# Optimization experiments

Measured on AMD Instinct MI355X. Metric: run time of the kernel, lower is better.

Reference implementation:

```python
import jax, jax.numpy as jnp
import numpy as np

D_IN = 1024
D_OUT = 1024
N_HEADS = 16
D_HEAD = D_OUT // N_HEADS


def setup_inputs() -> dict:
    key = jax.random.key(0)
    ks = jax.random.split(key, 6)
    s = 0.02
    return {
        "x": jax.random.normal(ks[0], (4, 2048, D_IN), dtype=jnp.float32),
        "wq": jax.random.normal(ks[1], (D_IN, D_OUT), dtype=jnp.float32) * s,
        "wk": jax.random.normal(ks[2], (D_IN, D_OUT), dtype=jnp.float32) * s,
        "wv": jax.random.normal(ks[3], (D_IN, D_OUT), dtype=jnp.float32) * s,
        "wo": jax.random.normal(ks[4], (D_OUT, D_OUT), dtype=jnp.float32) * s,
        "bo": jax.random.normal(ks[5], (D_OUT,), dtype=jnp.float32) * s,
    }


def reference(x, wq, wk, wv, wo, bo):
    B, T, _ = x.shape
    # QKV projections (no bias), split into heads: (B, H, T, Dh)
    def split_heads(t):
        return t.reshape(B, T, N_HEADS, D_HEAD).transpose(0, 2, 1, 3)
    q = split_heads(x @ wq)
    k = split_heads(x @ wk)
    v = split_heads(x @ wv)
    # attention scores (B, H, T, T), causal mask, scale by sqrt(d_head)
    scores = jnp.einsum("bhqd,bhkd->bhqk", q, k)
    causal = jnp.tril(jnp.ones((T, T), dtype=bool))
    scores = jnp.where(causal, scores, -jnp.inf)
    attn = jax.nn.softmax(scores / jnp.sqrt(jnp.float32(D_HEAD)), axis=-1)
    # dropout = 0.0 (eval) -> identity
    ctx = jnp.einsum("bhqk,bhkd->bhqd", attn, v)
    ctx = ctx.transpose(0, 2, 1, 3).reshape(B, T, D_OUT)
    return ctx @ wo + bo
```

## Files before the change

### kernel.cpp

```cpp
#include <hip/hip_runtime.h>
#include <stdint.h>


typedef unsigned short u16;
typedef __bf16 bf16x8 __attribute__((ext_vector_type(8)));
typedef float f32x4 __attribute__((ext_vector_type(4)));

__device__ __forceinline__ u16 f2bf(float f) {
  union { float f; unsigned u; } v; v.f = f;
  return (u16)((v.u + 0x7fffu + ((v.u >> 16) & 1u)) >> 16);
}

__device__ __forceinline__ void gl_lds16(const void* g, void* l) {
  __builtin_amdgcn_global_load_lds((__attribute__((address_space(1))) void*)g,
                                   (__attribute__((address_space(3))) void*)l,
                                   16, 0, 0);
}

__global__ __launch_bounds__(256) void conv_x_k(const float* __restrict__ x,
                                                u16* __restrict__ xb) {
  int i = (blockIdx.x * 256 + threadIdx.x) * 4;
  float4 v = *reinterpret_cast<const float4*>(x + i);
  ushort4 o;
  o.x = f2bf(v.x); o.y = f2bf(v.y); o.z = f2bf(v.z); o.w = f2bf(v.w);
  *reinterpret_cast<ushort4*>(xb + i) = o;
}

__global__ __launch_bounds__(256) void conv_w_k(const float* __restrict__ w0,
                                                const float* __restrict__ w1,
                                                const float* __restrict__ w2,
                                                const float* __restrict__ w3,
                                                u16* __restrict__ dst) {
  const float* src = blockIdx.z == 0 ? w0 : blockIdx.z == 1 ? w1
                   : blockIdx.z == 2 ? w2 : w3;
  u16* d = dst + (size_t)blockIdx.z * 1024 * 1024;
  __shared__ float tile[32][33];
  int n0 = blockIdx.x * 32, k0 = blockIdx.y * 32;
  int tx = threadIdx.x & 31, ty = threadIdx.x >> 5;
  #pragma unroll
  for (int r = 0; r < 32; r += 8)
    tile[ty + r][tx] = src[(k0 + ty + r) * 1024 + n0 + tx];
  __syncthreads();
  #pragma unroll
  for (int r = 0; r < 32; r += 8)
    d[(n0 + ty + r) * 1024 + k0 + tx] = f2bf(tile[tx][ty + r]);
}

#define GSW(base, row, chunk) \
  ((char*)(base) + (row) * 64 + ((((chunk) ^ (((row) >> 1) & 3))) << 4))

__global__ __launch_bounds__(256) void gemm_qkv_k(const u16* __restrict__ A,
                                                  const u16* __restrict__ Wt,
                                                  u16* __restrict__ qw,
                                                  u16* __restrict__ kw,
                                                  u16* __restrict__ vtw) {
  __shared__ u16 SM[16384];
  const int tid = threadIdx.x;
  const int wave = tid >> 6, lane = tid & 63;
  const int quad = lane >> 4, l15 = lane & 15;
  const int m0 = blockIdx.x * 128;
  const int which = blockIdx.y >> 3;
  const int n0 = (blockIdx.y & 7) * 128;
  const u16* Bt = Wt + which * (1024 * 1024);
  const int waveM = (wave >> 1) * 64, waveN = (wave & 1) * 64;

  const f32x4 fz = {0.f, 0.f, 0.f, 0.f};
  f32x4 acc[4][4];
  #pragma unroll
  for (int i = 0; i < 4; i++)
    #pragma unroll
    for (int j = 0; j < 4; j++) acc[i][j] = fz;

  const int grow = tid >> 2;
  const int gsw8 = (((tid & 3) ^ ((grow >> 1) & 3)) * 8);
  const u16* Ag = A + (m0 + grow) * 1024 + gsw8;
  const u16* Bg = Bt + (n0 + grow) * 1024 + gsw8;

  {
    char* AsB = (char*)&SM[0] + wave * 1024;
    char* BsB = (char*)&SM[8192] + wave * 1024;
    gl_lds16(Ag, AsB);       gl_lds16(Ag + 65536, AsB + 4096);
    gl_lds16(Bg, BsB);       gl_lds16(Bg + 65536, BsB + 4096);
  }

  for (int s = 0; s < 32; s++) {
    const int cur = (s & 1) * 4096;
    __syncthreads();
    if (s < 31) {
      const int k0 = (s + 1) * 32;
      const int nxt = 4096 - cur;
      char* AsB = (char*)&SM[nxt] + wave * 1024;
      char* BsB = (char*)&SM[8192 + nxt] + wave * 1024;
      gl_lds16(Ag + k0, AsB);      gl_lds16(Ag + 65536 + k0, AsB + 4096);
      gl_lds16(Bg + k0, BsB);      gl_lds16(Bg + 65536 + k0, BsB + 4096);
    }
    bf16x8 af[4], bf[4];
    #pragma unroll
    for (int mi = 0; mi < 4; mi++)
      af[mi] = *reinterpret_cast<const bf16x8*>(GSW(&SM[cur], waveM + mi * 16 + l15, quad));
    #pragma unroll
    for (int ni = 0; ni < 4; ni++)
      bf[ni] = *reinterpret_cast<const bf16x8*>(GSW(&SM[8192 + cur], waveN + ni * 16 + l15, quad));
    #pragma unroll
    for (int mi = 0; mi < 4; mi++)
      #pragma unroll
      for (int ni = 0; ni < 4; ni++)
        acc[mi][ni] = __builtin_amdgcn_mfma_f32_16x16x32_bf16(af[mi], bf[ni], acc[mi][ni], 0, 0, 0);
  }

  if (which != 2) {
    #pragma unroll
    for (int mi = 0; mi < 4; mi++) {
      #pragma unroll
      for (int r = 0; r < 4; r++) {
        int m = m0 + waveM + mi * 16 + quad * 4 + r;
        int b = m >> 11, t = m & 2047;
        #pragma unroll
        for (int ni = 0; ni < 4; ni++) {
          int n = n0 + waveN + ni * 16 + l15;
          int h = n >> 6, d = n & 63;
          float v = acc[mi][ni][r];
          if (which == 0) qw[((b * 16 + h) * 2048 + t) * 64 + d] = f2bf(v * 0.125f);
          else            kw[((b * 16 + h) * 2048 + t) * 64 + d] = f2bf(v);
        }
      }
    }
  } else {
    __syncthreads();
    #pragma unroll
    for (int mi = 0; mi < 4; mi++)
      #pragma unroll
      for (int r = 0; r < 4; r++) {
        int ml = waveM + mi * 16 + quad * 4 + r;
        #pragma unroll
        for (int ni = 0; ni < 4; ni++) {
          int nl = waveN + ni * 16 + l15;
          int byte = nl * 256 + (((ml >> 3) ^ (nl & 7)) << 4) + (ml & 7) * 2;
          *(u16*)((char*)SM + byte) = f2bf(acc[mi][ni][r]);
        }
      }
    __syncthreads();
    const int b = m0 >> 11, t0 = m0 & 2047;
    #pragma unroll
    for (int i = 0; i < 8; i++) {
      int cid = tid + 256 * i;
      int nl = cid >> 4, tc = cid & 15;
      bf16x8 vv = *reinterpret_cast<const bf16x8*>(
          (char*)SM + nl * 256 + ((tc ^ (nl & 7)) << 4));
      int n = n0 + nl;
      int h = n >> 6, d = n & 63;
      *reinterpret_cast<bf16x8*>(vtw + (((b * 16 + h) * 64 + d) * 2048 + t0 + tc * 8)) = vv;
    }
  }
}

__global__ __launch_bounds__(256) void attn_k(const u16* __restrict__ Q,
                                              const u16* __restrict__ K,
                                              const u16* __restrict__ Vt,
                                              u16* __restrict__ ctx) {
  __shared__ u16 QPs[64 * 64];
  __shared__ u16 Ks[2][64 * 64];
  __shared__ u16 Vs[2][64 * 64];
  const int tid = threadIdx.x;
  const int wave = tid >> 6, lane = tid & 63;
  const int quad = lane >> 4, l15 = lane & 15;
  const int bh = blockIdx.x;
  const int qt = 31 - (int)blockIdx.y;
  const int b = bh >> 4, h = bh & 15;

  const u16* Qg = Q + (bh * 2048 + qt * 64) * 64;
  const u16* Kg = K + bh * (2048 * 64);
  const u16* Vg = Vt + bh * (64 * 2048);

  const int lrow = tid >> 3;
  const int lsw = ((tid & 7) ^ (lrow & 7)) * 8;

  gl_lds16(Qg + lrow * 64 + lsw, (char*)QPs + wave * 1024);
  gl_lds16(Qg + (32 + lrow) * 64 + lsw, (char*)QPs + wave * 1024 + 4096);
  {
    char* KsB = (char*)Ks[0] + wave * 1024;
    char* VsB = (char*)Vs[0] + wave * 1024;
    gl_lds16(Kg + lrow * 64 + lsw, KsB);
    gl_lds16(Kg + (32 + lrow) * 64 + lsw, KsB + 4096);
    gl_lds16(Vg + lrow * 2048 + lsw, VsB);
    gl_lds16(Vg + (32 + lrow) * 2048 + lsw, VsB + 4096);
  }

  bf16x8 onesb;
  #pragma unroll
  for (int i = 0; i < 8; i++) onesb[i] = (__bf16)1.0f;

  const f32x4 fz = {0.f, 0.f, 0.f, 0.f};
  f32x4 accO[4];
  f32x4 accL = fz;
  #pragma unroll
  for (int dt = 0; dt < 4; dt++) accO[dt] = fz;
  bf16x8 qf[2];

  #define SWZB(row, chunk) ((row) * 128 + (((chunk) ^ ((row) & 7)) << 4))

  for (int j = 0; j <= qt; j++) {
    const int cur = j & 1;
    __syncthreads();
    if (j < qt) {
      char* KsB = (char*)Ks[cur ^ 1] + wave * 1024;
      char* VsB = (char*)Vs[cur ^ 1] + wave * 1024;
      const int jr = (j + 1) * 64;
      gl_lds16(Kg + (jr + lrow) * 64 + lsw, KsB);
      gl_lds16(Kg + (jr + 32 + lrow) * 64 + lsw, KsB + 4096);
      gl_lds16(Vg + lrow * 2048 + jr + lsw, VsB);
      gl_lds16(Vg + (32 + lrow) * 2048 + jr + lsw, VsB + 4096);
    }
    if (j == 0) {
      #pragma unroll
      for (int kk = 0; kk < 2; kk++)
        qf[kk] = *reinterpret_cast<const bf16x8*>(
            (char*)QPs + SWZB(wave * 16 + l15, kk * 4 + quad));
    }

    f32x4 s[4];
    #pragma unroll
    for (int nt = 0; nt < 4; nt++) s[nt] = fz;
    #pragma unroll
    for (int kk = 0; kk < 2; kk++)
      #pragma unroll
      for (int nt = 0; nt < 4; nt++) {
        bf16x8 kf = *reinterpret_cast<const bf16x8*>(
            (char*)Ks[cur] + SWZB(nt * 16 + l15, kk * 4 + quad));
        s[nt] = __builtin_amdgcn_mfma_f32_16x16x32_bf16(qf[kk], kf, s[nt], 0, 0, 0);
      }

    if (j == qt) {
      #pragma unroll
      for (int nt = 0; nt < 4; nt++) {
        int col = nt * 16 + l15;
        int row0 = wave * 16 + quad * 4;
        #pragma unroll
        for (int r = 0; r < 4; r++)
          if (col > row0 + r) s[nt][r] = -1e30f;
      }
    }

    #pragma unroll
    for (int nt = 0; nt < 4; nt++)
      #pragma unroll
      for (int r = 0; r < 4; r++) {
        int prow = wave * 16 + quad * 4 + r;
        int pcol = nt * 16 + l15;
        int byte = prow * 128 + ((((pcol >> 3) ^ (prow & 7))) << 4) + (pcol & 7) * 2;
        *(u16*)((char*)QPs + byte) = f2bf(__expf(s[nt][r]));
      }
    __asm__ volatile("s_waitcnt lgkmcnt(0)" ::: "memory");

    #pragma unroll
    for (int kk = 0; kk < 2; kk++) {
      bf16x8 pf = *reinterpret_cast<const bf16x8*>(
          (char*)QPs + SWZB(wave * 16 + l15, kk * 4 + quad));
      accL = __builtin_amdgcn_mfma_f32_16x16x32_bf16(pf, onesb, accL, 0, 0, 0);
      #pragma unroll
      for (int dt = 0; dt < 4; dt++) {
        bf16x8 vf = *reinterpret_cast<const bf16x8*>(
            (char*)Vs[cur] + SWZB(dt * 16 + l15, kk * 4 + quad));
        accO[dt] = __builtin_amdgcn_mfma_f32_16x16x32_bf16(pf, vf, accO[dt], 0, 0, 0);
      }
    }
  }
  #undef SWZB

  float inv[4];
  #pragma unroll
  for (int r = 0; r < 4; r++) inv[r] = 1.0f / accL[r];
  const int trow = qt * 64 + wave * 16 + quad * 4;
  #pragma unroll
  for (int dt = 0; dt < 4; dt++)
    #pragma unroll
    for (int r = 0; r < 4; r++)
      ctx[(b * 2048 + trow + r) * 1024 + h * 64 + dt * 16 + l15] =
          f2bf(accO[dt][r] * inv[r]);
}

__global__ __launch_bounds__(256) void gemm_out_k(const u16* __restrict__ A,
                                                  const u16* __restrict__ Wt,
                                                  const float* __restrict__ bo,
                                                  float* __restrict__ out) {
  __shared__ u16 SM[16384];
  const int tid = threadIdx.x;
  const int wave = tid >> 6, lane = tid & 63;
  const int quad = lane >> 4, l15 = lane & 15;
  const int m0 = blockIdx.x * 128;
  const int n0 = blockIdx.y * 128;
  const int waveM = (wave >> 1) * 64, waveN = (wave & 1) * 64;

  const f32x4 fz = {0.f, 0.f, 0.f, 0.f};
  f32x4 acc[4][4];
  #pragma unroll
  for (int i = 0; i < 4; i++)
    #pragma unroll
    for (int j = 0; j < 4; j++) acc[i][j] = fz;

  const int grow = tid >> 2;
  const int gsw8 = (((tid & 3) ^ ((grow >> 1) & 3)) * 8);
  const u16* Ag = A + (m0 + grow) * 1024 + gsw8;
  const u16* Bg = Wt + (n0 + grow) * 1024 + gsw8;

  {
    char* AsB = (char*)&SM[0] + wave * 1024;
    char* BsB = (char*)&SM[8192] + wave * 1024;
    gl_lds16(Ag, AsB);       gl_lds16(Ag + 65536, AsB + 4096);
    gl_lds16(Bg, BsB);       gl_lds16(Bg + 65536, BsB + 4096);
  }

  for (int s = 0; s < 32; s++) {
    const int cur = (s & 1) * 4096;
    __syncthreads();
    if (s < 31) {
      const int k0 = (s + 1) * 32;
      const int nxt = 4096 - cur;
      char* AsB = (char*)&SM[nxt] + wave * 1024;
      char* BsB = (char*)&SM[8192 + nxt] + wave * 1024;
      gl_lds16(Ag + k0, AsB);      gl_lds16(Ag + 65536 + k0, AsB + 4096);
      gl_lds16(Bg + k0, BsB);      gl_lds16(Bg + 65536 + k0, BsB + 4096);
    }
    bf16x8 af[4], bf[4];
    #pragma unroll
    for (int mi = 0; mi < 4; mi++)
      af[mi] = *reinterpret_cast<const bf16x8*>(GSW(&SM[cur], waveM + mi * 16 + l15, quad));
    #pragma unroll
    for (int ni = 0; ni < 4; ni++)
      bf[ni] = *reinterpret_cast<const bf16x8*>(GSW(&SM[8192 + cur], waveN + ni * 16 + l15, quad));
    #pragma unroll
    for (int mi = 0; mi < 4; mi++)
      #pragma unroll
      for (int ni = 0; ni < 4; ni++)
        acc[mi][ni] = __builtin_amdgcn_mfma_f32_16x16x32_bf16(af[mi], bf[ni], acc[mi][ni], 0, 0, 0);
  }
  float bias[4];
  #pragma unroll
  for (int ni = 0; ni < 4; ni++) bias[ni] = bo[n0 + waveN + ni * 16 + l15];
  #pragma unroll
  for (int mi = 0; mi < 4; mi++)
    #pragma unroll
    for (int r = 0; r < 4; r++) {
      int m = m0 + waveM + mi * 16 + quad * 4 + r;
      #pragma unroll
      for (int ni = 0; ni < 4; ni++) {
        int n = n0 + waveN + ni * 16 + l15;
        out[(size_t)m * 1024 + n] = acc[mi][ni][r] + bias[ni];
      }
    }
}

extern "C" void kernel_launch(void* const* d_in, const int* in_sizes, int n_in,
                              void* d_out, int out_size, void* d_ws, size_t ws_size,
                              hipStream_t stream) {
  const float* x  = (const float*)d_in[0];
  const float* wq = (const float*)d_in[1];
  const float* wk = (const float*)d_in[2];
  const float* wv = (const float*)d_in[3];
  const float* wo = (const float*)d_in[4];
  const float* bo = (const float*)d_in[5];
  float* out = (float*)d_out;
  char* ws = (char*)d_ws;

  u16* xb  = (u16*)(ws);
  u16* wt  = (u16*)(ws + 16777216);
  u16* qw  = (u16*)(ws + 25165824);
  u16* kw  = (u16*)(ws + 41943040);
  u16* vtw = (u16*)(ws + 58720256);

  conv_x_k<<<8192, 256, 0, stream>>>(x, xb);
  conv_w_k<<<dim3(32, 32, 4), 256, 0, stream>>>(wq, wk, wv, wo, wt);
  gemm_qkv_k<<<dim3(64, 24), 256, 0, stream>>>(xb, wt, qw, kw, vtw);
  attn_k<<<dim3(64, 32), 256, 0, stream>>>(qw, kw, vtw, xb );
  gemm_out_k<<<dim3(64, 8), 256, 0, stream>>>(xb, wt + 3 * 1024 * 1024, bo, out);
}
```

Before: 254.5 us.

## Keep attention probabilities in registers via transposed S MFMA and 16x16x16 PV

```diff
diff --git a/kernel.cpp b/kernel.cpp
--- a/kernel.cpp
+++ b/kernel.cpp
@@ -4,6 +4,7 @@
 
 typedef unsigned short u16;
 typedef __bf16 bf16x8 __attribute__((ext_vector_type(8)));
+typedef short s16x4 __attribute__((ext_vector_type(4)));
 typedef float f32x4 __attribute__((ext_vector_type(4)));
 
 __device__ __forceinline__ u16 f2bf(float f) {
@@ -158,7 +159,7 @@
                                               const u16* __restrict__ K,
                                               const u16* __restrict__ Vt,
                                               u16* __restrict__ ctx) {
-  __shared__ u16 QPs[64 * 64];
+  __shared__ u16 Qs[64 * 64];
   __shared__ u16 Ks[2][64 * 64];
   __shared__ u16 Vs[2][64 * 64];
   const int tid = threadIdx.x;
@@ -175,8 +176,8 @@
   const int lrow = tid >> 3;
   const int lsw = ((tid & 7) ^ (lrow & 7)) * 8;
 
-  gl_lds16(Qg + lrow * 64 + lsw, (char*)QPs + wave * 1024);
-  gl_lds16(Qg + (32 + lrow) * 64 + lsw, (char*)QPs + wave * 1024 + 4096);
+  gl_lds16(Qg + lrow * 64 + lsw, (char*)Qs + wave * 1024);
+  gl_lds16(Qg + (32 + lrow) * 64 + lsw, (char*)Qs + wave * 1024 + 4096);
   {
     char* KsB = (char*)Ks[0] + wave * 1024;
     char* VsB = (char*)Vs[0] + wave * 1024;
@@ -186,10 +187,7 @@
     gl_lds16(Vg + (32 + lrow) * 2048 + lsw, VsB + 4096);
   }
 
-  bf16x8 onesb;
-  #pragma unroll
-  for (int i = 0; i < 8; i++) onesb[i] = (__bf16)1.0f;
-
+  const s16x4 ones4 = {(short)0x3F80, (short)0x3F80, (short)0x3F80, (short)0x3F80};
   const f32x4 fz = {0.f, 0.f, 0.f, 0.f};
   f32x4 accO[4];
   f32x4 accL = fz;
@@ -215,7 +213,7 @@
       #pragma unroll
       for (int kk = 0; kk < 2; kk++)
         qf[kk] = *reinterpret_cast<const bf16x8*>(
-            (char*)QPs + SWZB(wave * 16 + l15, kk * 4 + quad));
+            (char*)Qs + SWZB(wave * 16 + l15, kk * 4 + quad));
     }
 
     f32x4 s[4];
@@ -227,41 +225,41 @@
       for (int nt = 0; nt < 4; nt++) {
         bf16x8 kf = *reinterpret_cast<const bf16x8*>(
             (char*)Ks[cur] + SWZB(nt * 16 + l15, kk * 4 + quad));
-        s[nt] = __builtin_amdgcn_mfma_f32_16x16x32_bf16(qf[kk], kf, s[nt], 0, 0, 0);
+        s[nt] = __builtin_amdgcn_mfma_f32_16x16x32_bf16(kf, qf[kk], s[nt], 0, 0, 0);
       }
 
     if (j == qt) {
-      #pragma unroll
-      for (int nt = 0; nt < 4; nt++) {
-        int col = nt * 16 + l15;
-        int row0 = wave * 16 + quad * 4;
+      const int qrow = wave * 16 + l15;
+      #pragma unroll
+      for (int nt = 0; nt < 4; nt++)
         #pragma unroll
         for (int r = 0; r < 4; r++)
-          if (col > row0 + r) s[nt][r] = -1e30f;
-      }
-    }
-
-    #pragma unroll
-    for (int nt = 0; nt < 4; nt++)
-      #pragma unroll
-      for (int r = 0; r < 4; r++) {
-        int prow = wave * 16 + quad * 4 + r;
-        int pcol = nt * 16 + l15;
-        int byte = prow * 128 + ((((pcol >> 3) ^ (prow & 7))) << 4) + (pcol & 7) * 2;
-        *(u16*)((char*)QPs + byte) = f2bf(__expf(s[nt][r]));
-      }
-    __asm__ volatile("s_waitcnt lgkmcnt(0)" ::: "memory");
-
-    #pragma unroll
-    for (int kk = 0; kk < 2; kk++) {
-      bf16x8 pf = *reinterpret_cast<const bf16x8*>(
-          (char*)QPs + SWZB(wave * 16 + l15, kk * 4 + quad));
-      accL = __builtin_amdgcn_mfma_f32_16x16x32_bf16(pf, onesb, accL, 0, 0, 0);
+          if (nt * 16 + quad * 4 + r > qrow) s[nt][r] = -1e30f;
+    }
+
+    s16x4 pf[4];
+    #pragma unroll
+    for (int nt = 0; nt < 4; nt++) {
+      float p0 = __expf(s[nt][0]), p1 = __expf(s[nt][1]);
+      float p2 = __expf(s[nt][2]), p3 = __expf(s[nt][3]);
+      union { s16x4 v; unsigned u[2]; } pk;
+      pk.u[0] = __builtin_amdgcn_perm(__float_as_uint(p1), __float_as_uint(p0),
+                                      0x07060302u);
+      pk.u[1] = __builtin_amdgcn_perm(__float_as_uint(p3), __float_as_uint(p2),
+                                      0x07060302u);
+      pf[nt] = pk.v;
+    }
+
+    #pragma unroll
+    for (int kc = 0; kc < 4; kc++) {
+      accL = __builtin_amdgcn_mfma_f32_16x16x16bf16_1k(pf[kc], ones4, accL, 0, 0, 0);
       #pragma unroll
       for (int dt = 0; dt < 4; dt++) {
-        bf16x8 vf = *reinterpret_cast<const bf16x8*>(
-            (char*)Vs[cur] + SWZB(dt * 16 + l15, kk * 4 + quad));
-        accO[dt] = __builtin_amdgcn_mfma_f32_16x16x32_bf16(pf, vf, accO[dt], 0, 0, 0);
+        int row = dt * 16 + l15;
+        int byte = row * 128 + (((kc * 2 + (quad >> 1)) ^ (l15 & 7)) << 4) +
+                   (quad & 1) * 8;
+        s16x4 vf = *reinterpret_cast<const s16x4*>((char*)Vs[cur] + byte);
+        accO[dt] = __builtin_amdgcn_mfma_f32_16x16x16bf16_1k(pf[kc], vf, accO[dt], 0, 0, 0);
       }
     }
   }
```

Measured after the change: 252.6 us. About the same (-0.8%).
